# Kernel optimization log

Hardware: AMD Instinct MI355X
Metric: run time of the kernel (lower is better)

## Reference

```python
import jax, jax.numpy as jnp
import numpy as np
from jax import lax

B, FMAP, ENC, DEC, ATTN = 64, 512, 256, 512, 256
NUM_CLASSES, MAX_LEN = 96, 30
H, W = 8, 32


def setup_inputs() -> dict:
    key = jax.random.key(0)
    ks = jax.random.split(key, 20)
    s = 0.02
    inp = {
        "feature_map": jax.random.normal(ks[0], (B, FMAP, H, W), jnp.float32),
        "h0": jax.random.normal(ks[1], (2, B, DEC), jnp.float32),
        "c0": jax.random.normal(ks[2], (2, B, DEC), jnp.float32),
        "target": jax.random.randint(ks[3], (B, MAX_LEN), 0, NUM_CLASSES),
        "length": jax.random.randint(ks[4], (B,), 1, MAX_LEN),
        # embedding table: (num_classes+1, enc_dim)
        "emb": jax.random.normal(ks[5], (NUM_CLASSES + 1, ENC), jnp.float32) * s,
        # LSTM layer 0 (input ENC -> DEC), PyTorch gate order i,f,g,o
        "Wih0": jax.random.normal(ks[6], (4 * DEC, ENC), jnp.float32) * s,
        "Whh0": jax.random.normal(ks[7], (4 * DEC, DEC), jnp.float32) * s,
        "bih0": jnp.zeros((4 * DEC,), jnp.float32),
        "bhh0": jnp.zeros((4 * DEC,), jnp.float32),
        # LSTM layer 1 (DEC -> DEC)
        "Wih1": jax.random.normal(ks[8], (4 * DEC, DEC), jnp.float32) * s,
        "Whh1": jax.random.normal(ks[9], (4 * DEC, DEC), jnp.float32) * s,
        "bih1": jnp.zeros((4 * DEC,), jnp.float32),
        "bhh1": jnp.zeros((4 * DEC,), jnp.float32),
        # attention convs: 1x1 on hidden -> linear; 3x3 on fmap; 1x1 attn->1
        "e_lstm_w": jax.random.normal(ks[10], (ATTN, DEC), jnp.float32) * s,
        "e_lstm_b": jnp.zeros((ATTN,), jnp.float32),
        "e_fmap_w": jax.random.normal(ks[11], (ATTN, FMAP, 3, 3), jnp.float32) * s,
        "e_fmap_b": jnp.zeros((ATTN,), jnp.float32),
        "a_w": jax.random.normal(ks[12], (1, ATTN), jnp.float32) * s,
        "a_b": jnp.zeros((1,), jnp.float32),
        # fc: (dec+fmap) -> num_classes+2
        "fc_w": jax.random.normal(ks[13], (NUM_CLASSES + 2, DEC + FMAP), jnp.float32) * s,
        "fc_b": jnp.zeros((NUM_CLASSES + 2,), jnp.float32),
    }
    return inp


def _lstm_cell(x, h, c, Wih, Whh, bih, bhh):
    gates = x @ Wih.T + h @ Whh.T + (bih + bhh)
    i, f, g, o = jnp.split(gates, 4, axis=-1)
    i, f, o = jax.nn.sigmoid(i), jax.nn.sigmoid(f), jax.nn.sigmoid(o)
    c = f * c + i * jnp.tanh(g)
    h = o * jnp.tanh(c)
    return h, c


def reference(feature_map, h0, c0, target, length, emb,
              Wih0, Whh0, bih0, bhh0, Wih1, Whh1, bih1, bhh1,
              e_lstm_w, e_lstm_b, e_fmap_w, e_fmap_b, a_w, a_b, fc_w, fc_b):
    del length  # unused in forward math
    batch = feature_map.shape[0]
    # precompute 3x3 conv on the (constant) feature map once: [B, ATTN, H, W]
    e_fmap = lax.conv_general_dilated(
        feature_map, e_fmap_w, window_strides=(1, 1), padding="SAME",
        dimension_numbers=("NCHW", "OIHW", "NCHW")) + e_fmap_b[None, :, None, None]

    # teacher-forced input sequence: BOS token 0 then target -> [T+1, B]
    labels = jnp.concatenate(
        [jnp.zeros((batch, 1), target.dtype), target], axis=1).T  # [T+1, B]
    emb_seq = emb[labels]  # [T+1, B, ENC]

    def step(carry, x_t):
        h0_, c0_, h1_, c1_ = carry
        h0_, c0_ = _lstm_cell(x_t, h0_, c0_, Wih0, Whh0, bih0, bhh0)
        h1_, c1_ = _lstm_cell(h0_, h1_, c1_, Wih1, Whh1, bih1, bhh1)
        # additive conv attention
        e_h = h1_ @ e_lstm_w.T + e_lstm_b  # [B, ATTN]
        e = jnp.tanh(e_h[:, :, None, None] + e_fmap)  # [B, ATTN, H, W]
        score = jnp.einsum("bahw,a->bhw", e, a_w[0]) + a_b[0]  # [B, H, W]
        a = jax.nn.softmax(score.reshape(batch, -1), axis=-1)
        mask = a.reshape(batch, *score.shape[1:])  # [B, H, W]
        glimpse = jnp.einsum("bchw,bhw->bc", feature_map, mask)  # [B, FMAP]
        logit = jnp.concatenate([h1_, glimpse], axis=-1) @ fc_w.T + fc_b
        return (h0_, c0_, h1_, c1_), (logit, mask, glimpse)

    carry0 = (h0[0], c0[0], h0[1], c0[1])
    _, (logits, masks, glimpses) = lax.scan(step, carry0, emb_seq)
    # time-major -> batch-major
    logits = jnp.transpose(logits, (1, 0, 2))      # [B, T+1, C+2]
    masks = jnp.transpose(masks, (1, 0, 2, 3))     # [B, T+1, H, W]
    glimpses = jnp.transpose(glimpses, (1, 0, 2))  # [B, T+1, FMAP]
    return logits, masks, glimpses
```

## Files before the change

kernel.cpp:

```cpp
#include <hip/hip_runtime.h>
#include <hip/hip_bf16.h>


typedef __bf16 bf16_8 __attribute__((ext_vector_type(8)));
typedef __bf16 bf16_4 __attribute__((ext_vector_type(4)));
typedef __bf16 bf16_2 __attribute__((ext_vector_type(2)));
typedef float f32x4 __attribute__((ext_vector_type(4)));

typedef __hip_bfloat16 bf;

__device__ __forceinline__ float b2f(bf h) { return __bfloat162float(h); }
__device__ __forceinline__ bf f2b(float f) { return __float2bfloat16(f); }
__device__ __forceinline__ float sigm(float x) { return 1.0f / (1.0f + __expf(-x)); }
__device__ __forceinline__ float tanh_f(float x) { return 1.0f - 2.0f / (1.0f + __expf(2.0f * x)); }
__device__ __forceinline__ f32x4 mfma16(bf16_8 a, bf16_8 b, f32x4 c) {
    return __builtin_amdgcn_mfma_f32_16x16x32_bf16(a, b, c, 0, 0, 0);
}

#define NB 64
#define FMAP 512
#define ENC 256
#define DEC 512
#define ATTN 256
#define NC2 98
#define TT 31
#define HW 256
#define NROWS 1984


__global__ void k_detect(const int* __restrict__ t32, int* __restrict__ flags) {
    __shared__ int i64f;
    int tid = threadIdx.x;
    if (tid == 0) i64f = 1;
    __syncthreads();
    for (int i = tid; i < 960; i += 256)
        if (t32[2 * i + 1] != 0) i64f = 0;
    __syncthreads();
    if (tid == 0) { flags[0] = 0; flags[1] = i64f; }
}

#define N_CVT 17
struct CvtTab {
    const void* src[N_CVT];
    unsigned long long off[N_CVT];
    int n[N_CVT];
};

__global__ void k_cvt(CvtTab tab, unsigned char* __restrict__ ws) {
    int id = blockIdx.y;
    int n = tab.n[id];
    bf* dst = (bf*)(ws + tab.off[id]);
    const float* sf = (const float*)tab.src[id];
    for (int i = blockIdx.x * 256 + threadIdx.x; i < n; i += 256 * gridDim.x)
        dst[i] = f2b(sf[i]);
}


__global__ void k_init_state(const float* __restrict__ h0, const float* __restrict__ c0,
                             bf* __restrict__ h0b, bf* __restrict__ h1_all,
                             float* __restrict__ c0f, float* __restrict__ c1f) {
    int i = blockIdx.x * 256 + threadIdx.x;
    if (i >= NB * DEC) return;
    h0b[32768 + i] = f2b(h0[i]);
    h1_all[i] = f2b(h0[NB * DEC + i]);
    c0f[i] = c0[i];
    c1f[i] = c0[NB * DEC + i];
}

__global__ void k_embed(const int* __restrict__ target, const bf* __restrict__ emb,
                        bf* __restrict__ x_seq, const int* __restrict__ flags) {
    int t = blockIdx.x, b = blockIdx.y, e = threadIdx.x;
    int lab = 0;
    if (t > 0) {
        int idx = b * 30 + (t - 1);
        lab = flags[1] ? target[2 * idx] : target[idx];
    }
    lab = min(max(lab, 0), 96);
    x_seq[(t * NB + b) * ENC + e] = emb[lab * ENC + e];
}

__global__ void k_wt(const bf* __restrict__ ew, bf* __restrict__ wt) {
    int dydx = blockIdx.x, a = blockIdx.y;
    for (int c = threadIdx.x; c < FMAP; c += 256)
        wt[(dydx * ATTN + a) * FMAP + c] = ew[(a * FMAP + c) * 9 + dydx];
}

__global__ __launch_bounds__(256) void k_padT(const float* __restrict__ fmapf,
                                              bf* __restrict__ fmapT) {
    __shared__ bf T3[64 * 258];
    int b = blockIdx.x, cq = blockIdx.y;
    int tid = threadIdx.x;
    for (int c_l = 0; c_l < 64; c_l++) {
        float v = fmapf[((size_t)(b * FMAP + cq * 64 + c_l)) * HW + tid];
        T3[c_l * 258 + tid] = f2b(v);
    }
    __syncthreads();
    int c_o = tid & 63, pg = tid >> 6;
    for (int it = 0; it < 64; it++) {
        int pos = it * 4 + pg;
        fmapT[((size_t)b * HW + pos) * FMAP + cq * 64 + c_o] = T3[c_o * 258 + pos];
    }
}

__global__ __launch_bounds__(256) void k_conv(const bf* __restrict__ fmapT,
                                              const bf* __restrict__ wt,
                                              const bf* __restrict__ efb,
                                              bf* __restrict__ ef) {
    __shared__ __align__(16) bf T[257 * 72];
    int b = blockIdx.x, aHalf = blockIdx.y, pQ = blockIdx.z;
    int tid = threadIdx.x, wv = tid >> 6, lane = tid & 63;
    int q = lane >> 4, l = lane & 15;
    int abase = aHalf * 128 + wv * 32;

    for (int i = tid; i < 72; i += 256) T[256 * 72 + i] = f2b(0.0f);

    const bf* pb = fmapT + (size_t)b * HW * FMAP;
    f32x4 acc[2][4] = {};
    for (int cQ = 0; cQ < 8; cQ++) {
        __syncthreads();
#pragma unroll
        for (int j = 0; j < 8; j++) {
            int chunk = j * 256 + tid;
            int row = chunk >> 3, g = chunk & 7;
            *(bf16_8*)(T + row * 72 + g * 8) =
                *(const bf16_8*)(pb + (size_t)row * FMAP + cQ * 64 + g * 8);
        }
        __syncthreads();
        for (int dydx = 0; dydx < 9; dydx++) {
            int dy = dydx / 3, dx = dydx % 3;
            int rowv[4];
#pragma unroll
            for (int nt = 0; nt < 4; nt++) {
                int y = pQ * 2 + (nt >> 1);
                int yp = y + dy - 1;
                int x = (nt & 1) * 16 + l;
                int xp = x + dx - 1;
                bool ok = (yp >= 0 && yp < 8 && xp >= 0 && xp < 32);
                rowv[nt] = ok ? (yp * 32 + xp) : 256;
            }
            const bf* wtd = wt + ((size_t)dydx * ATTN) * FMAP;
#pragma unroll
            for (int ck = 0; ck < 2; ck++) {
                int kg = cQ * 64 + ck * 32 + q * 8;
                bf16_8 afr[2];
#pragma unroll
                for (int mt = 0; mt < 2; mt++)
                    afr[mt] = *(const bf16_8*)(wtd + (abase + mt * 16 + l) * FMAP + kg);
#pragma unroll
                for (int nt = 0; nt < 4; nt++) {
                    bf16_8 bfr = *(const bf16_8*)(T + rowv[nt] * 72 + ck * 32 + q * 8);
                    acc[0][nt] = mfma16(afr[0], bfr, acc[0][nt]);
                    acc[1][nt] = mfma16(afr[1], bfr, acc[1][nt]);
                }
            }
        }
    }
#pragma unroll
    for (int mt = 0; mt < 2; mt++)
#pragma unroll
        for (int nt = 0; nt < 4; nt++) {
            int a0 = abase + mt * 16 + q * 4;
            int pos = pQ * 64 + nt * 16 + l;
            bf16_4 o;
#pragma unroll
            for (int r = 0; r < 4; r++) o[r] = f2b(acc[mt][nt][r] + b2f(efb[a0 + r]));
            *(bf16_4*)(ef + ((size_t)(b * HW + pos)) * ATTN + a0) = o;
        }
}


__global__ __launch_bounds__(512) void k_lstm(
        int s,
        const bf* __restrict__ x_seq,
        const bf* __restrict__ Wih0, const bf* __restrict__ Whh0,
        const bf* __restrict__ bih0, const bf* __restrict__ bhh0,
        const bf* __restrict__ Wih1, const bf* __restrict__ Whh1,
        const bf* __restrict__ bih1, const bf* __restrict__ bhh1,
        bf* __restrict__ h0b, bf* __restrict__ h1_all,
        float* __restrict__ c0f, float* __restrict__ c1f) {
    __shared__ f32x4 red4[4][4][64];
    const int blk = blockIdx.x, tid = threadIdx.x;
    const int wave = tid >> 6, lane = tid & 63;
    const int q = lane >> 4, l = lane & 15;
    const int kh = wave >> 2, bt = wave & 3;
    const int pcur = s & 1, pprev = (s + 1) & 1;
    const bool is0 = (blk >= 32);
    const int d0 = (is0 ? (blk - 32) : blk) * 16;
    const int d = d0 + l;

    f32x4 acc[4] = {};
    if (is0) {
        if (s > 30) return;
        const bf* xt = x_seq + (size_t)s * NB * ENC;
        const bf* hprev = h0b + pprev * 32768;
        if (kh == 0) {
#pragma unroll
            for (int k0 = 0; k0 < ENC; k0 += 32) {
                bf16_8 af = *(const bf16_8*)(xt + (bt * 16 + l) * ENC + k0 + q * 8);
#pragma unroll
                for (int g = 0; g < 4; g++) {
                    bf16_8 bfr = *(const bf16_8*)(Wih0 + (g * 512 + d0 + l) * ENC + k0 + q * 8);
                    acc[g] = mfma16(af, bfr, acc[g]);
                }
            }
        } else {
#pragma unroll 4
            for (int k0 = 0; k0 < DEC; k0 += 32) {
                bf16_8 af = *(const bf16_8*)(hprev + (bt * 16 + l) * DEC + k0 + q * 8);
#pragma unroll
                for (int g = 0; g < 4; g++) {
                    bf16_8 bfr = *(const bf16_8*)(Whh0 + (g * 512 + d0 + l) * DEC + k0 + q * 8);
                    acc[g] = mfma16(af, bfr, acc[g]);
                }
            }
#pragma unroll
            for (int g = 0; g < 4; g++) red4[bt][g][lane] = acc[g];
        }
        __syncthreads();
        if (kh == 0) {
            bf* hnew = h0b + pcur * 32768;
            float bi[4];
#pragma unroll
            for (int g = 0; g < 4; g++) {
                acc[g] += red4[bt][g][lane];
                bi[g] = b2f(bih0[g * 512 + d]) + b2f(bhh0[g * 512 + d]);
            }
#pragma unroll
            for (int r = 0; r < 4; r++) {
                int bb = bt * 16 + q * 4 + r;
                float gi = sigm(acc[0][r] + bi[0]);
                float gf = sigm(acc[1][r] + bi[1]);
                float gg = tanh_f(acc[2][r] + bi[2]);
                float go = sigm(acc[3][r] + bi[3]);
                float c = gf * c0f[bb * DEC + d] + gi * gg;
                c0f[bb * DEC + d] = c;
                hnew[bb * DEC + d] = f2b(go * tanh_f(c));
            }
        }
    } else {
        if (s < 1) return;
        const bf* h0n = h0b + pprev * 32768;
        const bf* h1p = h1_all + (size_t)(s - 1) * 32768;
        const bf* Ain = kh ? h1p : h0n;
        const bf* Wp  = kh ? Whh1 : Wih1;
#pragma unroll 4
        for (int k0 = 0; k0 < DEC; k0 += 32) {
            bf16_8 af = *(const bf16_8*)(Ain + (bt * 16 + l) * DEC + k0 + q * 8);
#pragma unroll
            for (int g = 0; g < 4; g++) {
                bf16_8 bfr = *(const bf16_8*)(Wp + (g * 512 + d0 + l) * DEC + k0 + q * 8);
                acc[g] = mfma16(af, bfr, acc[g]);
            }
        }
        if (kh == 1) {
#pragma unroll
            for (int g = 0; g < 4; g++) red4[bt][g][lane] = acc[g];
        }
        __syncthreads();
        if (kh == 0) {
            bf* h1n = h1_all + (size_t)s * 32768;
            float bi[4];
#pragma unroll
            for (int g = 0; g < 4; g++) {
                acc[g] += red4[bt][g][lane];
                bi[g] = b2f(bih1[g * 512 + d]) + b2f(bhh1[g * 512 + d]);
            }
#pragma unroll
            for (int r = 0; r < 4; r++) {
                int bb = bt * 16 + q * 4 + r;
                float gi = sigm(acc[0][r] + bi[0]);
                float gf = sigm(acc[1][r] + bi[1]);
                float gg = tanh_f(acc[2][r] + bi[2]);
                float go = sigm(acc[3][r] + bi[3]);
                float c = gf * c1f[bb * DEC + d] + gi * gg;
                c1f[bb * DEC + d] = c;
                h1n[bb * DEC + d] = f2b(go * tanh_f(c));
            }
        }
    }
}


__global__ __launch_bounds__(256) void k_eh(const bf* __restrict__ h1_all,
                                            const bf* __restrict__ ew,
                                            const bf* __restrict__ eb,
                                            float* __restrict__ EHf) {
    int mtile = blockIdx.x, ntile = blockIdx.y;
    int tid = threadIdx.x, wv = tid >> 6, lane = tid & 63;
    int q = lane >> 4, l = lane & 15;
    const bf* A = h1_all + 32768;
    f32x4 acc[4] = {};
    for (int k0 = 0; k0 < DEC; k0 += 32) {
        bf16_8 af = *(const bf16_8*)(A + (size_t)(mtile * 64 + wv * 16 + l) * DEC + k0 + q * 8);
#pragma unroll
        for (int g = 0; g < 4; g++) {
            bf16_8 bfr = *(const bf16_8*)(ew + (size_t)(ntile * 64 + g * 16 + l) * DEC + k0 + q * 8);
            acc[g] = mfma16(af, bfr, acc[g]);
        }
    }
#pragma unroll
    for (int g = 0; g < 4; g++) {
        int col = ntile * 64 + g * 16 + l;
        float bias = b2f(eb[col]);
#pragma unroll
        for (int r = 0; r < 4; r++) {
            int m = mtile * 64 + wv * 16 + q * 4 + r;
            EHf[(size_t)m * ATTN + col] = acc[g][r] + bias;
        }
    }
}

__global__ __launch_bounds__(256) void k_score(const float* __restrict__ EHf,
                                               const bf* __restrict__ ef,
                                               const bf* __restrict__ a_w,
                                               float* __restrict__ out_masks,
                                               bf* __restrict__ maskb) {
    __shared__ float ehs[ATTN];
    __shared__ float aws[ATTN];
    __shared__ float red[256];
    int b = blockIdx.x, t = blockIdx.y, tid = threadIdx.x;

    ehs[tid] = EHf[(size_t)(t * NB + b) * ATTN + tid];
    aws[tid] = b2f(a_w[tid]);
    __syncthreads();

    const bf16_8* er = (const bf16_8*)(ef + ((size_t)b * HW + tid) * ATTN);
    float s0 = 0.f, s1 = 0.f, s2 = 0.f, s3 = 0.f;
#pragma unroll 4
    for (int a8 = 0; a8 < ATTN / 8; a8++) {
        bf16_8 e8 = er[a8];
        int a = a8 * 8;
        s0 += aws[a + 0] * tanh_f(ehs[a + 0] + (float)e8[0]);
        s1 += aws[a + 1] * tanh_f(ehs[a + 1] + (float)e8[1]);
        s2 += aws[a + 2] * tanh_f(ehs[a + 2] + (float)e8[2]);
        s3 += aws[a + 3] * tanh_f(ehs[a + 3] + (float)e8[3]);
        s0 += aws[a + 4] * tanh_f(ehs[a + 4] + (float)e8[4]);
        s1 += aws[a + 5] * tanh_f(ehs[a + 5] + (float)e8[5]);
        s2 += aws[a + 6] * tanh_f(ehs[a + 6] + (float)e8[6]);
        s3 += aws[a + 7] * tanh_f(ehs[a + 7] + (float)e8[7]);
    }
    float sc = (s0 + s1) + (s2 + s3);
    red[tid] = sc;
    __syncthreads();
    for (int off = 128; off > 0; off >>= 1) {
        if (tid < off) red[tid] = fmaxf(red[tid], red[tid + off]);
        __syncthreads();
    }
    float mx = red[0];
    __syncthreads();
    float ex = __expf(sc - mx);
    red[tid] = ex;
    __syncthreads();
    for (int off = 128; off > 0; off >>= 1) {
        if (tid < off) red[tid] += red[tid + off];
        __syncthreads();
    }
    float mk = ex / red[0];
    out_masks[((size_t)b * TT + t) * HW + tid] = mk;
    maskb[((size_t)b * 32 + t) * HW + tid] = f2b(mk);
}

__global__ __launch_bounds__(256) void k_glimpse(const float* __restrict__ fmapf,
                                                 const bf* __restrict__ maskb,
                                                 float* __restrict__ out_glimpses,
                                                 bf* __restrict__ glb) {
    int b = blockIdx.x, ctile = blockIdx.y;
    int tid = threadIdx.x, wv = tid >> 6, lane = tid & 63;
    int q = lane >> 4, l = lane & 15;
    const float* A = fmapf + (size_t)b * FMAP * HW + (size_t)(ctile * 64 + wv * 16 + l) * HW;
    const bf* B = maskb + (size_t)b * 32 * HW;
    f32x4 acc[2] = {};
    for (int k0 = 0; k0 < HW; k0 += 32) {
        const float* ap = A + k0 + q * 8;
        f32x4 v0 = *(const f32x4*)(ap);
        f32x4 v1 = *(const f32x4*)(ap + 4);
        bf16_8 af;
#pragma unroll
        for (int j = 0; j < 4; j++) { af[j] = (__bf16)v0[j]; af[4 + j] = (__bf16)v1[j]; }
#pragma unroll
        for (int tt = 0; tt < 2; tt++) {
            bf16_8 bfr = *(const bf16_8*)(B + (size_t)(tt * 16 + l) * HW + k0 + q * 8);
            acc[tt] = mfma16(af, bfr, acc[tt]);
        }
    }
#pragma unroll
    for (int tt = 0; tt < 2; tt++) {
        int t = tt * 16 + l;
        if (t > 30) continue;
#pragma unroll
        for (int r = 0; r < 4; r++) {
            int c = ctile * 64 + wv * 16 + q * 4 + r;
            float g = acc[tt][r];
            out_glimpses[((size_t)b * TT + t) * FMAP + c] = g;
            glb[(size_t)(t * NB + b) * FMAP + c] = f2b(g);
        }
    }
}

__global__ __launch_bounds__(256) void k_logits(const bf* __restrict__ h1_all,
                                                const bf* __restrict__ glb,
                                                const bf* __restrict__ fc_w,
                                                const bf* __restrict__ fc_b,
                                                float* __restrict__ out_logits) {
    int mtile = blockIdx.x, ntile = blockIdx.y;
    int tid = threadIdx.x, wv = tid >> 6, lane = tid & 63;
    int q = lane >> 4, l = lane & 15;
    const bf* A1 = h1_all + 32768;
    int cls = ntile * 16 + l;
    int clsc = min(cls, NC2 - 1);
    int rowA = mtile * 64 + wv * 16 + l;
    f32x4 acc = {};
    for (int k0 = 0; k0 < 1024; k0 += 32) {
        bf16_8 af;
        if (k0 < DEC)
            af = *(const bf16_8*)(A1 + (size_t)rowA * DEC + k0 + q * 8);
        else
            af = *(const bf16_8*)(glb + (size_t)rowA * FMAP + (k0 - DEC) + q * 8);
        bf16_8 bfr = *(const bf16_8*)(fc_w + (size_t)clsc * (DEC + FMAP) + k0 + q * 8);
        acc = mfma16(af, bfr, acc);
    }
    if (cls < NC2) {
        float bias = b2f(fc_b[cls]);
#pragma unroll
        for (int r = 0; r < 4; r++) {
            int m = mtile * 64 + wv * 16 + q * 4 + r;
            int bb = m & 63, t = m >> 6;
            out_logits[((size_t)bb * TT + t) * NC2 + cls] = acc[r] + bias;
        }
    }
}


extern "C" void kernel_launch(void* const* d_in, const int* in_sizes, int n_in,
                              void* d_out, int out_size, void* d_ws, size_t ws_size,
                              hipStream_t stream) {
    float* out = (float*)d_out;
    float* out_logits   = out;
    float* out_masks    = out + 64 * 31 * 98;
    float* out_glimpses = out + 64 * 31 * (98 + 256);

    unsigned char* ws = (unsigned char*)d_ws;
    unsigned long long off = 0;
    auto carve = [&](size_t bytes) {
        unsigned long long o = off;
        off = (off + bytes + 15ULL) & ~15ULL;
        return o;
    };

    unsigned long long o_flags = carve(64);
    static const int cvt_in[N_CVT] = {5, 6, 7, 8, 9, 10, 11, 12, 13, 14, 15, 16, 17, 18, 19, 20, 21};
    static const int cvt_n[N_CVT] = {
        97 * 256, 2048 * 256, 2048 * 512, 2048, 2048,
        2048 * 512, 2048 * 512, 2048, 2048,
        256 * 512, 256, 256 * 512 * 9, 256, 256, 1,
        98 * 1024, 98
    };
    CvtTab tab;
    for (int i = 0; i < N_CVT; i++) {
        tab.src[i] = d_in[cvt_in[i]];
        tab.n[i] = cvt_n[i];
        tab.off[i] = carve((size_t)cvt_n[i] * 2);
    }
    const bf* emb_c    = (const bf*)(ws + tab.off[0]);
    const bf* Wih0_c   = (const bf*)(ws + tab.off[1]);
    const bf* Whh0_c   = (const bf*)(ws + tab.off[2]);
    const bf* bih0_c   = (const bf*)(ws + tab.off[3]);
    const bf* bhh0_c   = (const bf*)(ws + tab.off[4]);
    const bf* Wih1_c   = (const bf*)(ws + tab.off[5]);
    const bf* Whh1_c   = (const bf*)(ws + tab.off[6]);
    const bf* bih1_c   = (const bf*)(ws + tab.off[7]);
    const bf* bhh1_c   = (const bf*)(ws + tab.off[8]);
    const bf* e_lstm_w_c = (const bf*)(ws + tab.off[9]);
    const bf* e_lstm_b_c = (const bf*)(ws + tab.off[10]);
    const bf* e_fmap_w_c = (const bf*)(ws + tab.off[11]);
    const bf* e_fmap_b_c = (const bf*)(ws + tab.off[12]);
    const bf* a_w_c    = (const bf*)(ws + tab.off[13]);
    const bf* fc_w_c   = (const bf*)(ws + tab.off[15]);
    const bf* fc_b_c   = (const bf*)(ws + tab.off[16]);

    bf*    wt     = (bf*)(ws + carve((size_t)9 * 256 * 512 * 2));
    bf*    ef     = (bf*)(ws + carve((size_t)64 * 256 * 256 * 2));
    bf*    x_seq  = (bf*)(ws + carve((size_t)31 * 64 * 256 * 2));
    bf*    h0b    = (bf*)(ws + carve(2 * 65536));
    bf*    h1_all = (bf*)(ws + carve((size_t)32 * 65536));
    float* c0f    = (float*)(ws + carve(131072));
    float* c1f    = (float*)(ws + carve(131072));
    unsigned long long o_fmapT = carve((size_t)NB * HW * FMAP * 2);
    bf*    fmapT  = (bf*)(ws + o_fmapT);
    int*   flags  = (int*)(ws + o_flags);

    float* EHf    = (float*)(ws + o_fmapT);
    bf*    maskb  = (bf*)(ws + o_fmapT + 2031616ULL);
    bf*    glb    = (bf*)(ws + o_fmapT + 2031616ULL + 1048576ULL);

    k_detect<<<1, 256, 0, stream>>>((const int*)d_in[3], flags);
    k_cvt<<<dim3(256, N_CVT), 256, 0, stream>>>(tab, ws);
    k_init_state<<<128, 256, 0, stream>>>((const float*)d_in[1], (const float*)d_in[2],
                                          h0b, h1_all, c0f, c1f);
    k_embed<<<dim3(TT, NB), 256, 0, stream>>>((const int*)d_in[3], emb_c, x_seq, flags);
    k_wt<<<dim3(9, ATTN), 256, 0, stream>>>(e_fmap_w_c, wt);
    k_padT<<<dim3(NB, 8), 256, 0, stream>>>((const float*)d_in[0], fmapT);
    k_conv<<<dim3(NB, 2, 4), 256, 0, stream>>>(fmapT, wt, e_fmap_b_c, ef);

    for (int s = 0; s <= 31; s++)
        k_lstm<<<64, 512, 0, stream>>>(s, x_seq, Wih0_c, Whh0_c, bih0_c, bhh0_c,
                                       Wih1_c, Whh1_c, bih1_c, bhh1_c,
                                       h0b, h1_all, c0f, c1f);

    k_eh<<<dim3(31, 4), 256, 0, stream>>>(h1_all, e_lstm_w_c, e_lstm_b_c, EHf);
    k_score<<<dim3(NB, TT), 256, 0, stream>>>(EHf, ef, a_w_c, out_masks, maskb);
    k_glimpse<<<dim3(NB, 8), 256, 0, stream>>>((const float*)d_in[0], maskb,
                                               out_glimpses, glb);
    k_logits<<<dim3(31, 7), 256, 0, stream>>>(h1_all, glb, fc_w_c, fc_b_c, out_logits);
}
```

Before: 994.7 us.

## Fuse per-step LSTM launches into one cooperative kernel with grid barriers

Replaces 32 separate per-timestep LSTM kernel launches with a single cooperative kernel that loops over timesteps. Blocks synchronise through an atomic-counter grid barrier per step, and the counters are zeroed in the init kernel. This removes launch overhead and inter-kernel gaps on the serial recurrence, at the cost of spin-wait overhead and a bounded-spin guard that could break correctness if exceeded. The conv kernel is also retiled so each block covers 128 positions instead of 64, halving the grid and doubling register accumulators.

Result: slower. 1.238 ms (+24.4%).

```diff
diff --git a/kernel.cpp b/kernel.cpp
--- a/kernel.cpp
+++ b/kernel.cpp
@@ -4,7 +4,6 @@
 
 typedef __bf16 bf16_8 __attribute__((ext_vector_type(8)));
 typedef __bf16 bf16_4 __attribute__((ext_vector_type(4)));
-typedef __bf16 bf16_2 __attribute__((ext_vector_type(2)));
 typedef float f32x4 __attribute__((ext_vector_type(4)));
 
 typedef __hip_bfloat16 bf;
@@ -58,8 +57,10 @@
 
 __global__ void k_init_state(const float* __restrict__ h0, const float* __restrict__ c0,
                              bf* __restrict__ h0b, bf* __restrict__ h1_all,
-                             float* __restrict__ c0f, float* __restrict__ c1f) {
+                             float* __restrict__ c0f, float* __restrict__ c1f,
+                             int* __restrict__ bar) {
     int i = blockIdx.x * 256 + threadIdx.x;
+    if (blockIdx.x == 0 && threadIdx.x < 32) bar[threadIdx.x] = 0;
     if (i >= NB * DEC) return;
     h0b[32768 + i] = f2b(h0[i]);
     h1_all[i] = f2b(h0[NB * DEC + i]);
@@ -107,7 +108,7 @@
                                               const bf* __restrict__ efb,
                                               bf* __restrict__ ef) {
     __shared__ __align__(16) bf T[257 * 72];
-    int b = blockIdx.x, aHalf = blockIdx.y, pQ = blockIdx.z;
+    int b = blockIdx.x, aHalf = blockIdx.y, pHalf = blockIdx.z;
     int tid = threadIdx.x, wv = tid >> 6, lane = tid & 63;
     int q = lane >> 4, l = lane & 15;
     int abase = aHalf * 128 + wv * 32;
@@ -115,7 +116,7 @@
     for (int i = tid; i < 72; i += 256) T[256 * 72 + i] = f2b(0.0f);
 
     const bf* pb = fmapT + (size_t)b * HW * FMAP;
-    f32x4 acc[2][4] = {};
+    f32x4 acc[2][8] = {};
     for (int cQ = 0; cQ < 8; cQ++) {
         __syncthreads();
 #pragma unroll
@@ -128,10 +129,10 @@
         __syncthreads();
         for (int dydx = 0; dydx < 9; dydx++) {
             int dy = dydx / 3, dx = dydx % 3;
-            int rowv[4];
-#pragma unroll
-            for (int nt = 0; nt < 4; nt++) {
-                int y = pQ * 2 + (nt >> 1);
+            int rowv[8];
+#pragma unroll
+            for (int nt = 0; nt < 8; nt++) {
+                int y = pHalf * 4 + (nt >> 1);
                 int yp = y + dy - 1;
                 int x = (nt & 1) * 16 + l;
                 int xp = x + dx - 1;
@@ -147,7 +148,7 @@
                 for (int mt = 0; mt < 2; mt++)
                     afr[mt] = *(const bf16_8*)(wtd + (abase + mt * 16 + l) * FMAP + kg);
 #pragma unroll
-                for (int nt = 0; nt < 4; nt++) {
+                for (int nt = 0; nt < 8; nt++) {
                     bf16_8 bfr = *(const bf16_8*)(T + rowv[nt] * 72 + ck * 32 + q * 8);
                     acc[0][nt] = mfma16(afr[0], bfr, acc[0][nt]);
                     acc[1][nt] = mfma16(afr[1], bfr, acc[1][nt]);
@@ -158,9 +159,9 @@
 #pragma unroll
     for (int mt = 0; mt < 2; mt++)
 #pragma unroll
-        for (int nt = 0; nt < 4; nt++) {
+        for (int nt = 0; nt < 8; nt++) {
             int a0 = abase + mt * 16 + q * 4;
-            int pos = pQ * 64 + nt * 16 + l;
+            int pos = pHalf * 128 + nt * 16 + l;
             bf16_4 o;
 #pragma unroll
             for (int r = 0; r < 4; r++) o[r] = f2b(acc[mt][nt][r] + b2f(efb[a0 + r]));
@@ -169,114 +170,131 @@
 }
 
 
-__global__ __launch_bounds__(512) void k_lstm(
-        int s,
-        const bf* __restrict__ x_seq,
-        const bf* __restrict__ Wih0, const bf* __restrict__ Whh0,
-        const bf* __restrict__ bih0, const bf* __restrict__ bhh0,
-        const bf* __restrict__ Wih1, const bf* __restrict__ Whh1,
-        const bf* __restrict__ bih1, const bf* __restrict__ bhh1,
-        bf* __restrict__ h0b, bf* __restrict__ h1_all,
-        float* __restrict__ c0f, float* __restrict__ c1f) {
+struct SeqArgs {
+    const bf *x_seq, *Wih0, *Whh0, *bih0, *bhh0, *Wih1, *Whh1, *bih1, *bhh1;
+    bf *h0b, *h1_all;
+    float *c0f, *c1f;
+    int* bar;
+};
+
+__global__ __launch_bounds__(512) void k_seq(SeqArgs A) {
     __shared__ f32x4 red4[4][4][64];
     const int blk = blockIdx.x, tid = threadIdx.x;
     const int wave = tid >> 6, lane = tid & 63;
     const int q = lane >> 4, l = lane & 15;
     const int kh = wave >> 2, bt = wave & 3;
-    const int pcur = s & 1, pprev = (s + 1) & 1;
     const bool is0 = (blk >= 32);
     const int d0 = (is0 ? (blk - 32) : blk) * 16;
     const int d = d0 + l;
 
-    f32x4 acc[4] = {};
-    if (is0) {
-        if (s > 30) return;
-        const bf* xt = x_seq + (size_t)s * NB * ENC;
-        const bf* hprev = h0b + pprev * 32768;
-        if (kh == 0) {
-#pragma unroll
-            for (int k0 = 0; k0 < ENC; k0 += 32) {
-                bf16_8 af = *(const bf16_8*)(xt + (bt * 16 + l) * ENC + k0 + q * 8);
-#pragma unroll
-                for (int g = 0; g < 4; g++) {
-                    bf16_8 bfr = *(const bf16_8*)(Wih0 + (g * 512 + d0 + l) * ENC + k0 + q * 8);
-                    acc[g] = mfma16(af, bfr, acc[g]);
+    for (int s = 0; s <= 31; s++) {
+        const int pcur = s & 1, pprev = (s + 1) & 1;
+        if (is0) {
+            if (s <= 30) {
+                const bf* xt = A.x_seq + (size_t)s * NB * ENC;
+                const bf* hprev = A.h0b + pprev * 32768;
+                f32x4 acc[4] = {};
+                if (kh == 0) {
+#pragma unroll
+                    for (int k0 = 0; k0 < ENC; k0 += 32) {
+                        bf16_8 af = *(const bf16_8*)(xt + (bt * 16 + l) * ENC + k0 + q * 8);
+#pragma unroll
+                        for (int g = 0; g < 4; g++) {
+                            bf16_8 bfr = *(const bf16_8*)(A.Wih0 + (g * 512 + d0 + l) * ENC + k0 + q * 8);
+                            acc[g] = mfma16(af, bfr, acc[g]);
+                        }
+                    }
+                } else {
+#pragma unroll 4
+                    for (int k0 = 0; k0 < DEC; k0 += 32) {
+                        bf16_8 af = *(const bf16_8*)(hprev + (bt * 16 + l) * DEC + k0 + q * 8);
+#pragma unroll
+                        for (int g = 0; g < 4; g++) {
+                            bf16_8 bfr = *(const bf16_8*)(A.Whh0 + (g * 512 + d0 + l) * DEC + k0 + q * 8);
+                            acc[g] = mfma16(af, bfr, acc[g]);
+                        }
+                    }
+#pragma unroll
+                    for (int g = 0; g < 4; g++) red4[bt][g][lane] = acc[g];
+                }
+                __syncthreads();
+                if (kh == 0) {
+                    bf* hnew = A.h0b + pcur * 32768;
+                    float bi[4];
+#pragma unroll
+                    for (int g = 0; g < 4; g++) {
+                        acc[g] += red4[bt][g][lane];
+                        bi[g] = b2f(A.bih0[g * 512 + d]) + b2f(A.bhh0[g * 512 + d]);
+                    }
+#pragma unroll
+                    for (int r = 0; r < 4; r++) {
+                        int bb = bt * 16 + q * 4 + r;
+                        float gi = sigm(acc[0][r] + bi[0]);
+                        float gf = sigm(acc[1][r] + bi[1]);
+                        float gg = tanh_f(acc[2][r] + bi[2]);
+                        float go = sigm(acc[3][r] + bi[3]);
+                        float c = gf * A.c0f[bb * DEC + d] + gi * gg;
+                        A.c0f[bb * DEC + d] = c;
+                        hnew[bb * DEC + d] = f2b(go * tanh_f(c));
+                    }
                 }
             }
         } else {
+            if (s >= 1) {
+                const bf* h0n = A.h0b + pprev * 32768;
+                const bf* h1p = A.h1_all + (size_t)(s - 1) * 32768;
+                const bf* Ain = kh ? h1p : h0n;
+                const bf* Wp  = kh ? A.Whh1 : A.Wih1;
+                f32x4 acc[4] = {};
 #pragma unroll 4
-            for (int k0 = 0; k0 < DEC; k0 += 32) {
-                bf16_8 af = *(const bf16_8*)(hprev + (bt * 16 + l) * DEC + k0 + q * 8);
-#pragma unroll
-                for (int g = 0; g < 4; g++) {
-                    bf16_8 bfr = *(const bf16_8*)(Whh0 + (g * 512 + d0 + l) * DEC + k0 + q * 8);
-                    acc[g] = mfma16(af, bfr, acc[g]);
+                for (int k0 = 0; k0 < DEC; k0 += 32) {
+                    bf16_8 af = *(const bf16_8*)(Ain + (bt * 16 + l) * DEC + k0 + q * 8);
+#pragma unroll
+                    for (int g = 0; g < 4; g++) {
+                        bf16_8 bfr = *(const bf16_8*)(Wp + (g * 512 + d0 + l) * DEC + k0 + q * 8);
+                        acc[g] = mfma16(af, bfr, acc[g]);
+                    }
+                }
+                if (kh == 1) {
+#pragma unroll
+                    for (int g = 0; g < 4; g++) red4[bt][g][lane] = acc[g];
+                }
+                __syncthreads();
+                if (kh == 0) {
+                    bf* h1n = A.h1_all + (size_t)s * 32768;
+                    float bi[4];
+#pragma unroll
+                    for (int g = 0; g < 4; g++) {
+                        acc[g] += red4[bt][g][lane];
+                        bi[g] = b2f(A.bih1[g * 512 + d]) + b2f(A.bhh1[g * 512 + d]);
+                    }
+#pragma unroll
+                    for (int r = 0; r < 4; r++) {
+                        int bb = bt * 16 + q * 4 + r;
+                        float gi = sigm(acc[0][r] + bi[0]);
+                        float gf = sigm(acc[1][r] + bi[1]);
+                        float gg = tanh_f(acc[2][r] + bi[2]);
+                        float go = sigm(acc[3][r] + bi[3]);
+                        float c = gf * A.c1f[bb * DEC + d] + gi * gg;
+                        A.c1f[bb * DEC + d] = c;
+                        h1n[bb * DEC + d] = f2b(go * tanh_f(c));
+                    }
                 }
             }
-#pragma unroll
-            for (int g = 0; g < 4; g++) red4[bt][g][lane] = acc[g];
         }
         __syncthreads();
-        if (kh == 0) {
-            bf* hnew = h0b + pcur * 32768;
-            float bi[4];
-#pragma unroll
-            for (int g = 0; g < 4; g++) {
-                acc[g] += red4[bt][g][lane];
-                bi[g] = b2f(bih0[g * 512 + d]) + b2f(bhh0[g * 512 + d]);
+        if (tid == 0) {
+            __hip_atomic_fetch_add(&A.bar[s], 1, __ATOMIC_RELEASE,
+                                   __HIP_MEMORY_SCOPE_AGENT);
+            int guard = 0;
+            while (__hip_atomic_load(&A.bar[s], __ATOMIC_RELAXED,
+                                     __HIP_MEMORY_SCOPE_AGENT) < 64) {
+                __builtin_amdgcn_s_sleep(1);
+                if (++guard > (1 << 22)) break;
             }
-#pragma unroll
-            for (int r = 0; r < 4; r++) {
-                int bb = bt * 16 + q * 4 + r;
-                float gi = sigm(acc[0][r] + bi[0]);
-                float gf = sigm(acc[1][r] + bi[1]);
-                float gg = tanh_f(acc[2][r] + bi[2]);
-                float go = sigm(acc[3][r] + bi[3]);
-                float c = gf * c0f[bb * DEC + d] + gi * gg;
-                c0f[bb * DEC + d] = c;
-                hnew[bb * DEC + d] = f2b(go * tanh_f(c));
-            }
-        }
-    } else {
-        if (s < 1) return;
-        const bf* h0n = h0b + pprev * 32768;
-        const bf* h1p = h1_all + (size_t)(s - 1) * 32768;
-        const bf* Ain = kh ? h1p : h0n;
-        const bf* Wp  = kh ? Whh1 : Wih1;
-#pragma unroll 4
-        for (int k0 = 0; k0 < DEC; k0 += 32) {
-            bf16_8 af = *(const bf16_8*)(Ain + (bt * 16 + l) * DEC + k0 + q * 8);
-#pragma unroll
-            for (int g = 0; g < 4; g++) {
-                bf16_8 bfr = *(const bf16_8*)(Wp + (g * 512 + d0 + l) * DEC + k0 + q * 8);
-                acc[g] = mfma16(af, bfr, acc[g]);
-            }
-        }
-        if (kh == 1) {
-#pragma unroll
-            for (int g = 0; g < 4; g++) red4[bt][g][lane] = acc[g];
         }
         __syncthreads();
-        if (kh == 0) {
-            bf* h1n = h1_all + (size_t)s * 32768;
-            float bi[4];
-#pragma unroll
-            for (int g = 0; g < 4; g++) {
-                acc[g] += red4[bt][g][lane];
-                bi[g] = b2f(bih1[g * 512 + d]) + b2f(bhh1[g * 512 + d]);
-            }
-#pragma unroll
-            for (int r = 0; r < 4; r++) {
-                int bb = bt * 16 + q * 4 + r;
-                float gi = sigm(acc[0][r] + bi[0]);
-                float gf = sigm(acc[1][r] + bi[1]);
-                float gg = tanh_f(acc[2][r] + bi[2]);
-                float go = sigm(acc[3][r] + bi[3]);
-                float c = gf * c1f[bb * DEC + d] + gi * gg;
-                c1f[bb * DEC + d] = c;
-                h1n[bb * DEC + d] = f2b(go * tanh_f(c));
-            }
-        }
+        __builtin_amdgcn_fence(__ATOMIC_ACQUIRE, "agent");
     }
 }
 
@@ -448,6 +466,7 @@
     };
 
     unsigned long long o_flags = carve(64);
+    unsigned long long o_bar = carve(256);
     static const int cvt_in[N_CVT] = {5, 6, 7, 8, 9, 10, 11, 12, 13, 14, 15, 16, 17, 18, 19, 20, 21};
     static const int cvt_n[N_CVT] = {
         97 * 256, 2048 * 256, 2048 * 512, 2048, 2048,
@@ -488,6 +507,7 @@
     unsigned long long o_fmapT = carve((size_t)NB * HW * FMAP * 2);
     bf*    fmapT  = (bf*)(ws + o_fmapT);
     int*   flags  = (int*)(ws + o_flags);
+    int*   bar    = (int*)(ws + o_bar);
 
     float* EHf    = (float*)(ws + o_fmapT);
     bf*    maskb  = (bf*)(ws + o_fmapT + 2031616ULL);
@@ -496,16 +516,20 @@
     k_detect<<<1, 256, 0, stream>>>((const int*)d_in[3], flags);
     k_cvt<<<dim3(256, N_CVT), 256, 0, stream>>>(tab, ws);
     k_init_state<<<128, 256, 0, stream>>>((const float*)d_in[1], (const float*)d_in[2],
-                                          h0b, h1_all, c0f, c1f);
+                                          h0b, h1_all, c0f, c1f, bar);
     k_embed<<<dim3(TT, NB), 256, 0, stream>>>((const int*)d_in[3], emb_c, x_seq, flags);
     k_wt<<<dim3(9, ATTN), 256, 0, stream>>>(e_fmap_w_c, wt);
     k_padT<<<dim3(NB, 8), 256, 0, stream>>>((const float*)d_in[0], fmapT);
-    k_conv<<<dim3(NB, 2, 4), 256, 0, stream>>>(fmapT, wt, e_fmap_b_c, ef);
-
-    for (int s = 0; s <= 31; s++)
-        k_lstm<<<64, 512, 0, stream>>>(s, x_seq, Wih0_c, Whh0_c, bih0_c, bhh0_c,
-                                       Wih1_c, Whh1_c, bih1_c, bhh1_c,
-                                       h0b, h1_all, c0f, c1f);
+    k_conv<<<dim3(NB, 2, 2), 256, 0, stream>>>(fmapT, wt, e_fmap_b_c, ef);
+
+    SeqArgs qa;
+    qa.x_seq = x_seq; qa.Wih0 = Wih0_c; qa.Whh0 = Whh0_c;
+    qa.bih0 = bih0_c; qa.bhh0 = bhh0_c;
+    qa.Wih1 = Wih1_c; qa.Whh1 = Whh1_c; qa.bih1 = bih1_c; qa.bhh1 = bhh1_c;
+    qa.h0b = h0b; qa.h1_all = h1_all; qa.c0f = c0f; qa.c1f = c1f;
+    qa.bar = bar;
+    void* kargs[] = { (void*)&qa };
+    hipLaunchCooperativeKernel((const void*)k_seq, dim3(64), dim3(512), kargs, 0, stream);
 
     k_eh<<<dim3(31, 4), 256, 0, stream>>>(h1_all, e_lstm_w_c, e_lstm_b_c, EHf);
     k_score<<<dim3(NB, TT), 256, 0, stream>>>(EHf, ef, a_w_c, out_masks, maskb);
```
